# Kernel tuning notes

Hardware: AMD Instinct MI355X
Metric: run time of the kernel (lower is better)

Reference implementation:

```python
import jax, jax.numpy as jnp
import numpy as np

B, S, D, H = 2, 2048, 1024, 16
DK = D // H

def setup_inputs() -> dict:
    key = jax.random.key(0)
    ks = jax.random.split(key, 8)
    inp = {
        "Q": jax.random.normal(ks[0], (B, S, D), dtype=jnp.float32),
        "K": jax.random.normal(ks[1], (B, S, D), dtype=jnp.float32),
        "V": jax.random.normal(ks[2], (B, S, D), dtype=jnp.float32),
        "mask": jax.random.randint(ks[3], (B, 1, S, S), 0, 2, dtype=jnp.int32),
        # nn.Linear weights, shape [out_features, in_features], no bias
        "Wq": jax.random.normal(ks[4], (D, D), dtype=jnp.float32) / np.sqrt(D),
        "Wk": jax.random.normal(ks[5], (D, D), dtype=jnp.float32) / np.sqrt(D),
        "Wv": jax.random.normal(ks[6], (D, D), dtype=jnp.float32) / np.sqrt(D),
        "Wo": jax.random.normal(ks[7], (D, D), dtype=jnp.float32) / np.sqrt(D),
    }
    return inp

def reference(Q, K, V, mask, Wq, Wk, Wv, Wo):
    b, s, d = Q.shape
    # projections: y = x @ W.T (torch nn.Linear convention)
    q = (Q @ Wq.T).reshape(b, s, H, DK).transpose(0, 2, 1, 3)  # [b,h,s,dk]
    k = (K @ Wk.T).reshape(b, -1, H, DK).transpose(0, 2, 1, 3)
    v = (V @ Wv.T).reshape(b, -1, H, DK).transpose(0, 2, 1, 3)
    score = jnp.einsum("bhqd,bhkd->bhqk", q, k) / jnp.sqrt(jnp.float32(DK))
    # faithful to source: masked positions get value 1e-9 BEFORE softmax
    score = jnp.where(mask == 0, jnp.float32(1e-9), score)
    attn = jax.nn.softmax(score, axis=-1)
    # dropout p=0.1 treated as eval-mode identity
    out = jnp.einsum("bhqk,bhkd->bhqd", attn, v)  # [b,h,s,dk]
    out = out.transpose(0, 2, 1, 3).reshape(b, s, d)
    return out @ Wo.T
```

## Files before the change

kernel.cpp:

```cpp
#include <hip/hip_runtime.h>

typedef unsigned short u16;
typedef unsigned char  u8;
typedef unsigned long long u64;
typedef __attribute__((ext_vector_type(8))) short bf16x8;
typedef __attribute__((ext_vector_type(4))) float f32x4;

constexpr int B_  = 2;
constexpr int S_  = 2048;
constexpr int D_  = 1024;
constexpr int H_  = 16;
constexpr int DK_ = 64;
constexpr int NROW = B_ * S_;
constexpr size_t QSZ  = (size_t)B_ * H_ * S_ * DK_;
constexpr size_t XBSZ = (size_t)NROW * D_;
constexpr size_t WBSZ = (size_t)D_ * D_;
constexpr size_t MSZ  = (size_t)B_ * S_ * S_;
constexpr size_t MPKB = MSZ / 8;

__device__ __forceinline__ u16 f2bf(float f) {
    union { float f; unsigned u; } c; c.f = f;
    unsigned r = c.u + 0x7fffu + ((c.u >> 16) & 1u);
    return (u16)(r >> 16);
}
__device__ __forceinline__ unsigned pack2(float a, float b) {
    return (unsigned)f2bf(a) | ((unsigned)f2bf(b) << 16);
}
__device__ __forceinline__ unsigned cvt_pk_bf16(float a, float b) {
    unsigned r;
    asm("v_cvt_pk_bf16_f32 %0, %1, %2" : "=v"(r) : "v"(a), "v"(b));
    return r;
}

__device__ __forceinline__ void gl_lds16(const u16* g, u16* l) {
    __builtin_amdgcn_global_load_lds(
        (const __attribute__((address_space(1))) void*)g,
        (__attribute__((address_space(3))) void*)l, 16, 0, 0);
}

__global__ __launch_bounds__(256)
void cvt7m(const float* __restrict__ s0, const float* __restrict__ s1,
           const float* __restrict__ s2, const float* __restrict__ s3,
           const float* __restrict__ s4, const float* __restrict__ s5,
           const float* __restrict__ s6, const int* __restrict__ mk,
           u16* __restrict__ d0, u16* __restrict__ d1, u16* __restrict__ d2,
           u16* __restrict__ d3, u16* __restrict__ d4, u16* __restrict__ d5,
           u16* __restrict__ d6, u8* __restrict__ mp)
{
    constexpr size_t XT = 3 * XBSZ;
    constexpr int NCF = (int)((3 * XBSZ + 4 * WBSZ) / 2048);
    constexpr int NCM = (int)(MSZ / 2048);

    for (int c = blockIdx.x; c < NCF + NCM; c += gridDim.x) {
        if (c < NCF) {
            const size_t base = (size_t)c * 2048;
            const float* s; u16* d; size_t off;
            if (base < XT) {
                const int a = (int)(base >> 22);
                off = base & (XBSZ - 1);
                s = (a == 0) ? s0 : (a == 1) ? s1 : s2;
                d = (a == 0) ? d0 : (a == 1) ? d1 : d2;
            } else {
                const size_t r = base - XT;
                const int a = (int)(r >> 20);
                off = r & (WBSZ - 1);
                s = (a == 0) ? s3 : (a == 1) ? s4 : (a == 2) ? s5 : s6;
                d = (a == 0) ? d3 : (a == 1) ? d4 : (a == 2) ? d5 : d6;
            }
            const size_t e = off + (size_t)threadIdx.x * 8;
            const float4 x0 = *(const float4*)(s + e);
            const float4 x1 = *(const float4*)(s + e + 4);
            uint4 p;
            p.x = pack2(x0.x, x0.y); p.y = pack2(x0.z, x0.w);
            p.z = pack2(x1.x, x1.y); p.w = pack2(x1.z, x1.w);
            *(uint4*)(d + e) = p;
        } else {
            const size_t e = (size_t)(c - NCF) * 2048 + (size_t)threadIdx.x * 8;
            const int4 x0 = *(const int4*)(mk + e);
            const int4 x1 = *(const int4*)(mk + e + 4);
            unsigned bv = (unsigned)(x0.x != 0)        | ((unsigned)(x0.y != 0) << 1)
                        | ((unsigned)(x0.z != 0) << 2) | ((unsigned)(x0.w != 0) << 3)
                        | ((unsigned)(x1.x != 0) << 4) | ((unsigned)(x1.y != 0) << 5)
                        | ((unsigned)(x1.z != 0) << 6) | ((unsigned)(x1.w != 0) << 7);
            mp[e >> 3] = (u8)bv;
        }
    }
}

__global__ __launch_bounds__(256, 3)
void qkv_gemm2(const u16* __restrict__ Xq, const u16* __restrict__ Xk,
               const u16* __restrict__ Xv,
               const u16* __restrict__ Wq, const u16* __restrict__ Wk,
               const u16* __restrict__ Wv,
               u16* __restrict__ Yq, u16* __restrict__ Yk, u16* __restrict__ Yv)
{
    __shared__ u16 As[2 * 128 * 32];
    __shared__ u16 Bs[2 * 128 * 32];

    const int z = blockIdx.z;
    const u16* X = (z == 0) ? Xq : (z == 1) ? Xk : Xv;
    const u16* W = (z == 0) ? Wq : (z == 1) ? Wk : Wv;
    u16*       Y = (z == 0) ? Yq : (z == 1) ? Yk : Yv;
    const float osc = (z == 0) ? 0.125f : 1.0f;

    const int tid  = threadIdx.x;
    const int lane = tid & 63;
    const int w    = tid >> 6;
    const int quad = lane >> 4;
    const int lq   = lane & 15;
    const int wm   = (w & 1) << 6;
    const int wn   = (w >> 1) << 6;

    const int bid2 = (int)(blockIdx.x + (blockIdx.y << 5));
    const int swz2 = (bid2 & 7) * 32 + (bid2 >> 3);
    const int m0 = (swz2 & 31) << 7;
    const int n0 = (swz2 >> 5) << 7;

    const int srow = tid >> 2;
    const int scol = (tid & 3) << 3;
    const u16* ga0 = X + (size_t)(m0 + srow) * D_ + scol;
    const u16* ga1 = ga0 + (size_t)64 * D_;
    const u16* gb0 = W + (size_t)(n0 + srow) * D_ + scol;
    const u16* gb1 = gb0 + (size_t)64 * D_;

    const int wof = w << 9;

    f32x4 acc[4][4];
#pragma unroll
    for (int i = 0; i < 4; ++i)
#pragma unroll
        for (int j = 0; j < 4; ++j) acc[i][j] = (f32x4){0.f, 0.f, 0.f, 0.f};

    gl_lds16(ga0, As + wof);
    gl_lds16(ga1, As + 2048 + wof);
    gl_lds16(gb0, Bs + wof);
    gl_lds16(gb1, Bs + 2048 + wof);

    for (int kt = 0; kt < D_; kt += 32) {
        const int bi = (kt >> 5) & 1;
        const int bo = bi << 12;
        __syncthreads();
        if (kt + 32 < D_) {
            const int no = (bo ^ 4096);
            gl_lds16(ga0 + kt + 32, As + no + wof);
            gl_lds16(ga1 + kt + 32, As + no + 2048 + wof);
            gl_lds16(gb0 + kt + 32, Bs + no + wof);
            gl_lds16(gb1 + kt + 32, Bs + no + 2048 + wof);
        }

        bf16x8 af[4], bf[4];
#pragma unroll
        for (int t = 0; t < 4; ++t) {
            af[t] = *(const bf16x8*)&As[bo + (size_t)(wm + (t << 4) + lq) * 32 + (quad << 3)];
            bf[t] = *(const bf16x8*)&Bs[bo + (size_t)(wn + (t << 4) + lq) * 32 + (quad << 3)];
        }
#pragma unroll
        for (int i = 0; i < 4; ++i)
#pragma unroll
            for (int j = 0; j < 4; ++j)
                acc[i][j] = __builtin_amdgcn_mfma_f32_16x16x32_bf16(
                    af[i], bf[j], acc[i][j], 0, 0, 0);
    }

#pragma unroll
    for (int i = 0; i < 4; ++i)
#pragma unroll
        for (int j = 0; j < 4; ++j)
#pragma unroll
            for (int r = 0; r < 4; ++r) {
                const int grow = m0 + wm + (i << 4) + (quad << 2) + r;
                const int of   = n0 + wn + (j << 4) + lq;
                const int b = grow >> 11, s = grow & (S_ - 1);
                const int h = of >> 6,    dk = of & 63;
                Y[(((size_t)(b * H_ + h)) * S_ + s) * DK_ + dk] =
                    f2bf(acc[i][j][r] * osc);
            }
}

__global__ __launch_bounds__(256, 4)
void out_gemm2(const u16* __restrict__ X, const u16* __restrict__ W,
               float* __restrict__ Y)
{
    __shared__ u16 As[2 * 64 * 32];
    __shared__ u16 Bs[2 * 64 * 32];

    const int tid  = threadIdx.x;
    const int lane = tid & 63;
    const int w    = tid >> 6;
    const int quad = lane >> 4;
    const int lq   = lane & 15;
    const int wm   = (w & 1) << 5;
    const int wn   = (w >> 1) << 5;

    const int bid2 = (int)(blockIdx.x + (blockIdx.y << 6));
    const int swz2 = (bid2 & 7) * 128 + (bid2 >> 3);
    const int m0 = (swz2 & 63) << 6;
    const int n0 = (swz2 >> 6) << 6;

    const int srow = tid >> 2;
    const int scol = (tid & 3) << 3;
    const u16* ga0 = X + (size_t)(m0 + srow) * D_ + scol;
    const u16* gb0 = W + (size_t)(n0 + srow) * D_ + scol;

    const int wof = w << 9;

    f32x4 acc[2][2];
#pragma unroll
    for (int i = 0; i < 2; ++i)
#pragma unroll
        for (int j = 0; j < 2; ++j) acc[i][j] = (f32x4){0.f, 0.f, 0.f, 0.f};

    gl_lds16(ga0, As + wof);
    gl_lds16(gb0, Bs + wof);

    for (int kt = 0; kt < D_; kt += 32) {
        const int bi = (kt >> 5) & 1;
        const int bo = bi << 11;
        __syncthreads();
        if (kt + 32 < D_) {
            const int no = (bo ^ 2048);
            gl_lds16(ga0 + kt + 32, As + no + wof);
            gl_lds16(gb0 + kt + 32, Bs + no + wof);
        }

        bf16x8 af[2], bf[2];
#pragma unroll
        for (int t = 0; t < 2; ++t) {
            af[t] = *(const bf16x8*)&As[bo + (size_t)(wm + (t << 4) + lq) * 32 + (quad << 3)];
            bf[t] = *(const bf16x8*)&Bs[bo + (size_t)(wn + (t << 4) + lq) * 32 + (quad << 3)];
        }
#pragma unroll
        for (int i = 0; i < 2; ++i)
#pragma unroll
            for (int j = 0; j < 2; ++j)
                acc[i][j] = __builtin_amdgcn_mfma_f32_16x16x32_bf16(
                    af[i], bf[j], acc[i][j], 0, 0, 0);
    }

#pragma unroll
    for (int i = 0; i < 2; ++i)
#pragma unroll
        for (int j = 0; j < 2; ++j)
#pragma unroll
            for (int r = 0; r < 4; ++r) {
                const int grow = m0 + wm + (i << 4) + (quad << 2) + r;
                const int gcol = n0 + wn + (j << 4) + lq;
                Y[(size_t)grow * D_ + gcol] = acc[i][j][r];
            }
}

constexpr int AP = 72;

__global__ __launch_bounds__(256, 2)
void attn_mfma11(const u16* __restrict__ qb, const u16* __restrict__ kb,
                 const u16* __restrict__ vb, const u8* __restrict__ mpk,
                 u16* __restrict__ ctx)
{
    __shared__ u16 QPs[128][AP];
    __shared__ u16 Ks[2][64][AP];
    __shared__ u16 Vt[2][64][AP];

    const int tid  = threadIdx.x;
    const int lane = tid & 63;
    const int w    = tid >> 6;
    const int quad = lane >> 4;
    const int lq   = lane & 15;
    const int w32  = w << 5;

    const int bid = (int)(blockIdx.x + gridDim.x * (blockIdx.y + gridDim.y * blockIdx.z));
    const int swz = (bid & 7) * 64 + (bid >> 3);
    const int q0 = (swz & 15) << 7;
    const int h  = (swz >> 4) & 15;
    const int b  = swz >> 8;

    const u16* qbh = qb + (((size_t)b * H_ + h) * S_ + q0) * DK_;
    const u16* kbh = kb + ((size_t)b * H_ + h) * S_ * DK_;
    const u16* vbh = vb + ((size_t)b * H_ + h) * S_ * DK_;

    {
        const int r = tid >> 1, c = (tid & 1) << 5;
#pragma unroll
        for (int u = 0; u < 4; ++u)
            *(uint4*)&QPs[r][c + (u << 3)] =
                *(const uint4*)&qbh[(size_t)r * DK_ + c + (u << 3)];
    }
    __syncthreads();
    bf16x8 aQ[2][2];
#pragma unroll
    for (int i = 0; i < 2; ++i) {
        aQ[i][0] = *(const bf16x8*)&QPs[w32 + (i << 4) + lq][quad << 3];
        aQ[i][1] = *(const bf16x8*)&QPs[w32 + (i << 4) + lq][32 + (quad << 3)];
    }

    f32x4 O[2][4];
    float lsum[2][4];
#pragma unroll
    for (int i = 0; i < 2; ++i)
#pragma unroll
        for (int t = 0; t < 4; ++t) O[i][t] = (f32x4){0.f, 0.f, 0.f, 0.f};
#pragma unroll
    for (int i = 0; i < 2; ++i)
#pragma unroll
        for (int r = 0; r < 4; ++r) lsum[i][r] = 0.f;

    const int ksr = tid >> 2, ksc = (tid & 3) << 4;
    const int vc  = tid & 15;
    const int vs  = (tid >> 4) & 1;
    const int vk0 = vc + (vs << 5);
    const int vdg = tid >> 5;
    const int vcol = (vc << 2) + (vs << 1);

    uint4 kr0, kr1, vr0, vr1;
    {
        kr0 = *(const uint4*)&kbh[(size_t)ksr * DK_ + ksc];
        kr1 = *(const uint4*)&kbh[(size_t)ksr * DK_ + ksc + 8];
        vr0 = *(const uint4*)&vbh[(size_t)vk0 * DK_ + (vdg << 3)];
        vr1 = *(const uint4*)&vbh[(size_t)(vk0 + 16) * DK_ + (vdg << 3)];
    }

    const int qrow0 = q0 + w32 + (quad << 2);
    const u8* mrow = mpk + (size_t)b * S_ * (S_ / 8) + (size_t)qrow0 * (S_ / 8);

    for (int k0 = 0; k0 < S_; k0 += 64) {
        const int bi = (k0 >> 6) & 1;

        {
            *(uint4*)&Ks[bi][ksr][ksc]     = kr0;
            *(uint4*)&Ks[bi][ksr][ksc + 8] = kr1;
            const u16* a0 = (const u16*)&vr0;
            const u16* a1 = (const u16*)&vr1;
#pragma unroll
            for (int i = 0; i < 8; ++i)
                *(ushort2*)&Vt[bi][(vdg << 3) + i][vcol] = (ushort2){a0[i], a1[i]};
        }
        __syncthreads();

        if (k0 + 64 < S_) {
            const size_t kb0 = (size_t)(k0 + 64 + ksr) * DK_ + ksc;
            kr0 = *(const uint4*)&kbh[kb0];
            kr1 = *(const uint4*)&kbh[kb0 + 8];
            const size_t vb0 = (size_t)(k0 + 64 + vk0) * DK_ + (vdg << 3);
            vr0 = *(const uint4*)&vbh[vb0];
            vr1 = *(const uint4*)&vbh[vb0 + (size_t)16 * DK_];
        }

        u64 mw[2][4];
#pragma unroll
        for (int i = 0; i < 2; ++i)
#pragma unroll
            for (int r = 0; r < 4; ++r)
                mw[i][r] = *(const u64*)&mrow[(size_t)((i << 4) + r) * (S_ / 8) + (k0 >> 3)];

        f32x4 st[2][4];
#pragma unroll
        for (int t = 0; t < 4; ++t) {
            const bf16x8 b0 = *(const bf16x8*)&Ks[bi][(t << 4) + lq][quad << 3];
            const bf16x8 b1 = *(const bf16x8*)&Ks[bi][(t << 4) + lq][32 + (quad << 3)];
#pragma unroll
            for (int i = 0; i < 2; ++i) {
                f32x4 c = {0.f, 0.f, 0.f, 0.f};
                c = __builtin_amdgcn_mfma_f32_16x16x32_bf16(aQ[i][0], b0, c, 0, 0, 0);
                c = __builtin_amdgcn_mfma_f32_16x16x32_bf16(aQ[i][1], b1, c, 0, 0, 0);
                st[i][t] = c;
            }
        }

#pragma unroll
        for (int i = 0; i < 2; ++i)
#pragma unroll
            for (int r = 0; r < 4; ++r) {
                const unsigned lo = (unsigned)mw[i][r];
                const unsigned hi = (unsigned)(mw[i][r] >> 32);
                float p0 = __expf(st[i][0][r]);
                float p1 = __expf(st[i][1][r]);
                float p2 = __expf(st[i][2][r]);
                float p3 = __expf(st[i][3][r]);
                p0 = ((lo >> lq) & 1u) ? p0 : 1.0f;
                p1 = ((lo >> (lq + 16)) & 1u) ? p1 : 1.0f;
                p2 = ((hi >> lq) & 1u) ? p2 : 1.0f;
                p3 = ((hi >> (lq + 16)) & 1u) ? p3 : 1.0f;
                lsum[i][r] += (p0 + p1) + (p2 + p3);
                uint2 pw;
                pw.x = cvt_pk_bf16(p0, p1);
                pw.y = cvt_pk_bf16(p2, p3);
                *(uint2*)&QPs[w32 + (i << 4) + (quad << 2) + r][lq << 2] = pw;
            }

        bf16x8 aP[2][2];
#pragma unroll
        for (int i = 0; i < 2; ++i) {
            aP[i][0] = *(const bf16x8*)&QPs[w32 + (i << 4) + lq][quad << 3];
            aP[i][1] = *(const bf16x8*)&QPs[w32 + (i << 4) + lq][32 + (quad << 3)];
        }
#pragma unroll
        for (int t = 0; t < 4; ++t) {
            const bf16x8 b0 = *(const bf16x8*)&Vt[bi][(t << 4) + lq][quad << 3];
            const bf16x8 b1 = *(const bf16x8*)&Vt[bi][(t << 4) + lq][32 + (quad << 3)];
#pragma unroll
            for (int i = 0; i < 2; ++i) {
                O[i][t] = __builtin_amdgcn_mfma_f32_16x16x32_bf16(aP[i][0], b0, O[i][t], 0, 0, 0);
                O[i][t] = __builtin_amdgcn_mfma_f32_16x16x32_bf16(aP[i][1], b1, O[i][t], 0, 0, 0);
            }
        }
    }

#pragma unroll
    for (int i = 0; i < 2; ++i)
#pragma unroll
        for (int r = 0; r < 4; ++r) {
#pragma unroll
            for (int off = 1; off < 16; off <<= 1)
                lsum[i][r] += __shfl_xor(lsum[i][r], off);
            lsum[i][r] = 1.0f / lsum[i][r];
        }

#pragma unroll
    for (int i = 0; i < 2; ++i)
#pragma unroll
        for (int t = 0; t < 4; ++t)
#pragma unroll
            for (int r = 0; r < 4; ++r) {
                const int row = qrow0 + (i << 4) + r;
                ctx[((size_t)b * S_ + row) * D_ + (h << 6) + (t << 4) + lq] =
                    f2bf(O[i][t][r] * lsum[i][r]);
            }
}

extern "C" void kernel_launch(void* const* d_in, const int* in_sizes, int n_in,
                              void* d_out, int out_size, void* d_ws, size_t ws_size,
                              hipStream_t stream)
{
    const float* Q    = (const float*)d_in[0];
    const float* K    = (const float*)d_in[1];
    const float* V    = (const float*)d_in[2];
    const int*   mask = (const int*)d_in[3];
    const float* Wq   = (const float*)d_in[4];
    const float* Wk   = (const float*)d_in[5];
    const float* Wv   = (const float*)d_in[6];
    const float* Wo   = (const float*)d_in[7];
    float* out = (float*)d_out;

    u16* xqb = (u16*)d_ws;
    u16* xkb = xqb + XBSZ;
    u16* xvb = xqb + 2 * XBSZ;
    u16* wqb = xqb + 3 * XBSZ;
    u16* wkb = wqb + WBSZ;
    u16* wvb = wqb + 2 * WBSZ;
    u16* wob = wqb + 3 * WBSZ;
    u16* qw  = wqb + 4 * WBSZ;
    u16* kw  = qw + QSZ;
    u16* vw  = qw + 2 * QSZ;
    u8*  mpk = (u8*)(qw + 3 * QSZ);
    u16* cx  = xqb;

    hipLaunchKernelGGL(cvt7m, dim3(2048), dim3(256), 0, stream,
                       Q, K, V, Wq, Wk, Wv, Wo, mask,
                       xqb, xkb, xvb, wqb, wkb, wvb, wob, mpk);
    hipLaunchKernelGGL(qkv_gemm2, dim3(NROW / 128, D_ / 128, 3), dim3(256), 0, stream,
                       xqb, xkb, xvb, wqb, wkb, wvb, qw, kw, vw);
    hipLaunchKernelGGL(attn_mfma11, dim3(S_ / 128, H_, B_), dim3(256), 0, stream,
                       qw, kw, vw, mpk, cx);
    hipLaunchKernelGGL(out_gemm2, dim3(NROW / 64, D_ / 64), dim3(256), 0, stream,
                       cx, wob, out);
}
```

Measured before the change: 254.4 us.

## Move mask bit-packing from convert kernel into extra QKV GEMM grid slice

```diff
diff --git a/kernel.cpp b/kernel.cpp
--- a/kernel.cpp
+++ b/kernel.cpp
@@ -39,43 +39,61 @@
 }
 
 __global__ __launch_bounds__(256)
-void cvt7m(const float* __restrict__ s0, const float* __restrict__ s1,
+void cvt7x(const float* __restrict__ s0, const float* __restrict__ s1,
            const float* __restrict__ s2, const float* __restrict__ s3,
            const float* __restrict__ s4, const float* __restrict__ s5,
-           const float* __restrict__ s6, const int* __restrict__ mk,
+           const float* __restrict__ s6,
            u16* __restrict__ d0, u16* __restrict__ d1, u16* __restrict__ d2,
            u16* __restrict__ d3, u16* __restrict__ d4, u16* __restrict__ d5,
-           u16* __restrict__ d6, u8* __restrict__ mp)
+           u16* __restrict__ d6)
 {
     constexpr size_t XT = 3 * XBSZ;
     constexpr int NCF = (int)((3 * XBSZ + 4 * WBSZ) / 2048);
-    constexpr int NCM = (int)(MSZ / 2048);
-
-    for (int c = blockIdx.x; c < NCF + NCM; c += gridDim.x) {
-        if (c < NCF) {
-            const size_t base = (size_t)c * 2048;
-            const float* s; u16* d; size_t off;
-            if (base < XT) {
-                const int a = (int)(base >> 22);
-                off = base & (XBSZ - 1);
-                s = (a == 0) ? s0 : (a == 1) ? s1 : s2;
-                d = (a == 0) ? d0 : (a == 1) ? d1 : d2;
-            } else {
-                const size_t r = base - XT;
-                const int a = (int)(r >> 20);
-                off = r & (WBSZ - 1);
-                s = (a == 0) ? s3 : (a == 1) ? s4 : (a == 2) ? s5 : s6;
-                d = (a == 0) ? d3 : (a == 1) ? d4 : (a == 2) ? d5 : d6;
-            }
-            const size_t e = off + (size_t)threadIdx.x * 8;
-            const float4 x0 = *(const float4*)(s + e);
-            const float4 x1 = *(const float4*)(s + e + 4);
-            uint4 p;
-            p.x = pack2(x0.x, x0.y); p.y = pack2(x0.z, x0.w);
-            p.z = pack2(x1.x, x1.y); p.w = pack2(x1.z, x1.w);
-            *(uint4*)(d + e) = p;
+
+    for (int c = blockIdx.x; c < NCF; c += gridDim.x) {
+        const size_t base = (size_t)c * 2048;
+        const float* s; u16* d; size_t off;
+        if (base < XT) {
+            const int a = (int)(base >> 22);
+            off = base & (XBSZ - 1);
+            s = (a == 0) ? s0 : (a == 1) ? s1 : s2;
+            d = (a == 0) ? d0 : (a == 1) ? d1 : d2;
         } else {
-            const size_t e = (size_t)(c - NCF) * 2048 + (size_t)threadIdx.x * 8;
+            const size_t r = base - XT;
+            const int a = (int)(r >> 20);
+            off = r & (WBSZ - 1);
+            s = (a == 0) ? s3 : (a == 1) ? s4 : (a == 2) ? s5 : s6;
+            d = (a == 0) ? d3 : (a == 1) ? d4 : (a == 2) ? d5 : d6;
+        }
+        const size_t e = off + (size_t)threadIdx.x * 8;
+        const float4 x0 = *(const float4*)(s + e);
+        const float4 x1 = *(const float4*)(s + e + 4);
+        uint4 p;
+        p.x = pack2(x0.x, x0.y); p.y = pack2(x0.z, x0.w);
+        p.z = pack2(x1.x, x1.y); p.w = pack2(x1.z, x1.w);
+        *(uint4*)(d + e) = p;
+    }
+}
+
+__global__ __launch_bounds__(256, 3)
+void qkv_gemm3(const u16* __restrict__ Xq, const u16* __restrict__ Xk,
+               const u16* __restrict__ Xv,
+               const u16* __restrict__ Wq, const u16* __restrict__ Wk,
+               const u16* __restrict__ Wv,
+               const int* __restrict__ mk, u8* __restrict__ mp,
+               u16* __restrict__ Yq, u16* __restrict__ Yk, u16* __restrict__ Yv)
+{
+    __shared__ u16 As[2 * 128 * 32];
+    __shared__ u16 Bs[2 * 128 * 32];
+
+    const int z = blockIdx.z;
+    const int tid  = threadIdx.x;
+
+    if (z == 3) {
+        constexpr int NCM = (int)(MSZ / 2048);
+        const int b0 = (int)(blockIdx.x + (blockIdx.y << 5));
+        for (int c = b0; c < NCM; c += 256) {
+            const size_t e = (size_t)c * 2048 + (size_t)tid * 8;
             const int4 x0 = *(const int4*)(mk + e);
             const int4 x1 = *(const int4*)(mk + e + 4);
             unsigned bv = (unsigned)(x0.x != 0)        | ((unsigned)(x0.y != 0) << 1)
@@ -84,26 +102,14 @@
                         | ((unsigned)(x1.z != 0) << 6) | ((unsigned)(x1.w != 0) << 7);
             mp[e >> 3] = (u8)bv;
         }
-    }
-}
-
-__global__ __launch_bounds__(256, 3)
-void qkv_gemm2(const u16* __restrict__ Xq, const u16* __restrict__ Xk,
-               const u16* __restrict__ Xv,
-               const u16* __restrict__ Wq, const u16* __restrict__ Wk,
-               const u16* __restrict__ Wv,
-               u16* __restrict__ Yq, u16* __restrict__ Yk, u16* __restrict__ Yv)
-{
-    __shared__ u16 As[2 * 128 * 32];
-    __shared__ u16 Bs[2 * 128 * 32];
-
-    const int z = blockIdx.z;
+        return;
+    }
+
     const u16* X = (z == 0) ? Xq : (z == 1) ? Xk : Xv;
     const u16* W = (z == 0) ? Wq : (z == 1) ? Wk : Wv;
     u16*       Y = (z == 0) ? Yq : (z == 1) ? Yk : Yv;
     const float osc = (z == 0) ? 0.125f : 1.0f;
 
-    const int tid  = threadIdx.x;
     const int lane = tid & 63;
     const int w    = tid >> 6;
     const int quad = lane >> 4;
@@ -453,11 +459,11 @@
     u8*  mpk = (u8*)(qw + 3 * QSZ);
     u16* cx  = xqb;
 
-    hipLaunchKernelGGL(cvt7m, dim3(2048), dim3(256), 0, stream,
-                       Q, K, V, Wq, Wk, Wv, Wo, mask,
-                       xqb, xkb, xvb, wqb, wkb, wvb, wob, mpk);
-    hipLaunchKernelGGL(qkv_gemm2, dim3(NROW / 128, D_ / 128, 3), dim3(256), 0, stream,
-                       xqb, xkb, xvb, wqb, wkb, wvb, qw, kw, vw);
+    hipLaunchKernelGGL(cvt7x, dim3(2048), dim3(256), 0, stream,
+                       Q, K, V, Wq, Wk, Wv, Wo,
+                       xqb, xkb, xvb, wqb, wkb, wvb, wob);
+    hipLaunchKernelGGL(qkv_gemm3, dim3(NROW / 128, D_ / 128, 4), dim3(256), 0, stream,
+                       xqb, xkb, xvb, wqb, wkb, wvb, mask, mpk, qw, kw, vw);
     hipLaunchKernelGGL(attn_mfma11, dim3(S_ / 128, H_, B_), dim3(256), 0, stream,
                        qw, kw, vw, mpk, cx);
     hipLaunchKernelGGL(out_gemm2, dim3(NROW / 64, D_ / 64), dim3(256), 0, stream,
```

Measured after the change: 257.3 us. Within noise of the previous version (+1.2%).
